# Kernel optimization log

Hardware: AMD Instinct MI355X
Metric: run time of the kernel (lower is better)

The kernel has to match this reference:

```python
import jax, jax.numpy as jnp
import numpy as np

N_NODES = 50000
N_EDGES = 800000
HEADS = 4
OUT_CH = 32
EDGE_EMB = 4
NEG_SLOPE = 0.2


def setup_inputs() -> dict:
    key = jax.random.key(0)
    ks = jax.random.split(key, 6)
    x = jax.random.normal(ks[0], (N_NODES, 128), dtype=jnp.float32)
    edge_index = jax.random.randint(ks[1], (2, N_EDGES), 0, N_NODES, dtype=jnp.int32)
    edge_attr = jax.random.normal(ks[2], (N_EDGES, 8), dtype=jnp.float32)
    W = jax.random.normal(ks[3], (128, HEADS * OUT_CH), dtype=jnp.float32) * 0.08
    We = jax.random.normal(ks[4], (8, HEADS * EDGE_EMB), dtype=jnp.float32) * 0.3
    att = jax.random.normal(ks[5], (1, HEADS, 2 * OUT_CH + EDGE_EMB), dtype=jnp.float32) * 0.1
    bias = jnp.zeros((HEADS * OUT_CH,), dtype=jnp.float32)
    return {"x": x, "edge_index": edge_index, "edge_attr": edge_attr,
            "W": W, "We": We, "att": att, "bias": bias}


def reference(x, edge_index, edge_attr, W, We, att, bias):
    # x: [N, Din], edge_index: [2, E] (row 0 = source j, row 1 = target i)
    src = edge_index[0]
    dst = edge_index[1]
    n = x.shape[0]

    xh = (x @ W).reshape(n, HEADS, OUT_CH)                    # [N, H, O]
    eh = (edge_attr @ We).reshape(-1, HEADS, EDGE_EMB)        # [E, H, P]

    a_i = att[0, :, :OUT_CH]                                  # [H, O]
    a_j = att[0, :, OUT_CH:2 * OUT_CH]                        # [H, O]
    a_e = att[0, :, 2 * OUT_CH:]                              # [H, P]

    # per-node dot with att halves, then gather per edge (avoids [E,H,O] concat)
    s_i = jnp.einsum('nho,ho->nh', xh, a_i)                   # [N, H]
    s_j = jnp.einsum('nho,ho->nh', xh, a_j)                   # [N, H]
    s_e = jnp.einsum('ehp,hp->eh', eh, a_e)                   # [E, H]

    alpha = s_i[dst] + s_j[src] + s_e                         # [E, H]
    alpha = jax.nn.leaky_relu(alpha, NEG_SLOPE)

    # segment softmax over incoming edges of each target node
    m = jax.ops.segment_max(alpha, dst, num_segments=n)       # [N, H]
    m = jnp.where(jnp.isfinite(m), m, 0.0)
    ea = jnp.exp(alpha - m[dst])                              # [E, H]
    denom = jax.ops.segment_sum(ea, dst, num_segments=n)      # [N, H]
    alpha = ea / (denom[dst] + 1e-16)                         # [E, H]

    msg = xh[src] * alpha[:, :, None]                         # [E, H, O]
    aggr = jax.ops.segment_sum(msg, dst, num_segments=n)      # [N, H, O]
    out = aggr.reshape(n, HEADS * OUT_CH) + bias              # concat heads
    return out
```

## Files before the change

kernel.cpp:

```cpp
#include <hip/hip_runtime.h>
#include <hip/hip_fp16.h>
#include <stdint.h>
#include <math.h>

#define NEG_SLOPE 0.2f

static __device__ __forceinline__ unsigned short f2bf(float f) {
    unsigned u = __float_as_uint(f);
    unsigned r = (u + 0x7FFFu + ((u >> 16) & 1u)) >> 16;
    return (unsigned short)r;
}
static __device__ __forceinline__ unsigned pack_h2(float a, float b) {
    __half2 h = __floats2half2_rn(a, b);
    return *(unsigned*)&h;
}

__global__ __launch_bounds__(256, 4) void k_gemm_scatter(
    const float* __restrict__ x, const float* __restrict__ W,
    const float* __restrict__ att, unsigned short* __restrict__ xh16,
    float* __restrict__ s_i, float* __restrict__ s_j, int n, int GB,
    const int* __restrict__ ei, const float* __restrict__ edge_attr,
    const float* __restrict__ We, int* __restrict__ cnt, int4* __restrict__ bucket,
    int slots, int E) {
    if (blockIdx.x >= GB) {
        __shared__ float ceS[32];
        int t = threadIdx.x;
        if (t < 32) {
            int k = t >> 2, h = t & 3;
            float s = 0.f;
            #pragma unroll
            for (int p = 0; p < 4; ++p)
                s += We[k * 16 + h * 4 + p] * att[h * 68 + 64 + p];
            ceS[t] = s;
        }
        __syncthreads();
        int e = (blockIdx.x - GB) * 256 + t;
        if (e < E) {
            float4 ea0 = *(const float4*)(edge_attr + (size_t)e * 8);
            float4 ea1 = *(const float4*)(edge_attr + (size_t)e * 8 + 4);
            float eav[8] = {ea0.x, ea0.y, ea0.z, ea0.w, ea1.x, ea1.y, ea1.z, ea1.w};
            float se[4];
            #pragma unroll
            for (int h = 0; h < 4; ++h) {
                float s = 0.f;
                #pragma unroll
                for (int k = 0; k < 8; ++k) s += eav[k] * ceS[k * 4 + h];
                se[h] = s;
            }
            int src = ei[e], dst = ei[E + e];
            int4 ent;
            ent.x = src;
            ent.y = (int)pack_h2(se[0], se[1]);
            ent.z = (int)pack_h2(se[2], se[3]);
            ent.w = 0;
            int p = atomicAdd(&cnt[dst], 1);
            if (p < slots) bucket[(size_t)dst * slots + p] = ent;
        }
        return;
    }
    __shared__ float wS[32 * 128];
    __shared__ float xS[64 * 32];
    int t = threadIdx.x;
    int c4 = t & 31;
    int rg = t >> 5;
    int r0 = blockIdx.x * 64;

    float acc[8][4];
    #pragma unroll
    for (int r = 0; r < 8; ++r)
        #pragma unroll
        for (int j = 0; j < 4; ++j) acc[r][j] = 0.f;

    for (int ch = 0; ch < 4; ++ch) {
        {
            const float4* Wv = (const float4*)(W + (size_t)ch * 32 * 128);
            #pragma unroll
            for (int i = 0; i < 4; ++i)
                ((float4*)wS)[t + i * 256] = Wv[t + i * 256];
        }
        #pragma unroll
        for (int i = 0; i < 2; ++i) {
            int idx = t + i * 256;
            int r = idx >> 3;
            int q = idx & 7;
            int row = r0 + r;
            float4 v = make_float4(0.f, 0.f, 0.f, 0.f);
            if (row < n) v = *(const float4*)(x + (size_t)row * 128 + ch * 32 + q * 4);
            ((float4*)xS)[idx] = v;
        }
        __syncthreads();
        #pragma unroll 1
        for (int q = 0; q < 8; ++q) {
            float wv[4][4];
            #pragma unroll
            for (int kk = 0; kk < 4; ++kk)
                #pragma unroll
                for (int j = 0; j < 4; ++j)
                    wv[kk][j] = wS[(4 * q + kk) * 128 + 32 * j + c4];
            #pragma unroll
            for (int r = 0; r < 8; ++r) {
                float4 xv = ((const float4*)xS)[(rg * 8 + r) * 8 + q];
                #pragma unroll
                for (int j = 0; j < 4; ++j)
                    acc[r][j] += xv.x * wv[0][j] + xv.y * wv[1][j]
                               + xv.z * wv[2][j] + xv.w * wv[3][j];
            }
        }
        __syncthreads();
    }

    float ai[4], aj[4];
    #pragma unroll
    for (int j = 0; j < 4; ++j) {
        ai[j] = att[j * 68 + c4];
        aj[j] = att[j * 68 + 32 + c4];
    }
    #pragma unroll 1
    for (int r = 0; r < 8; ++r) {
        int row = r0 + rg * 8 + r;
        bool ok = row < n;
        if (ok) {
            #pragma unroll
            for (int j = 0; j < 4; ++j)
                xh16[(size_t)row * 128 + c4 + 32 * j] = f2bf(acc[r][j]);
        }
        float p[8];
        #pragma unroll
        for (int j = 0; j < 4; ++j) {
            p[j] = acc[r][j] * ai[j];
            p[4 + j] = acc[r][j] * aj[j];
        }
        #pragma unroll
        for (int m = 1; m < 32; m <<= 1) {
            #pragma unroll
            for (int i = 0; i < 8; ++i) p[i] += __shfl_xor(p[i], m);
        }
        if (c4 == 0 && ok) {
            *(float4*)(s_i + (size_t)row * 4) = make_float4(p[0], p[1], p[2], p[3]);
            *(float4*)(s_j + (size_t)row * 4) = make_float4(p[4], p[5], p[6], p[7]);
        }
    }
}

__global__ __launch_bounds__(256) void k_aggr(
    const int* __restrict__ cnt, const int4* __restrict__ bucket, int slots,
    const float* __restrict__ s_i, const float* __restrict__ s_j,
    const unsigned* __restrict__ xh32, const float* __restrict__ bias,
    float* __restrict__ out, int n) {
    __shared__ float wbuf[4][64][4];
    __shared__ int sbuf[4][64];
    int wid = threadIdx.x >> 6;
    int l = threadIdx.x & 63;
    int node = blockIdx.x * 4 + wid;
    if (node >= n) return;
    int deg = cnt[node];
    deg = deg < slots ? deg : slots;
    float2 b = ((const float2*)bias)[l];
    float2* op = (float2*)(out + (size_t)node * 128);
    if (deg == 0) { op[l] = b; return; }

    float4 si4 = *(const float4*)(s_i + (size_t)node * 4);
    float lg[4];
    int src = 0;
    bool valid = l < deg;
    if (valid) {
        int4 ent = bucket[(size_t)node * slots + l];
        src = ent.x;
        float4 sj4 = *(const float4*)(s_j + (size_t)src * 4);
        __half2 se01 = *(__half2*)&ent.y;
        __half2 se23 = *(__half2*)&ent.z;
        float2 se01f = __half22float2(se01);
        float2 se23f = __half22float2(se23);
        float a;
        a = si4.x + sj4.x + se01f.x; lg[0] = a > 0.f ? a : NEG_SLOPE * a;
        a = si4.y + sj4.y + se01f.y; lg[1] = a > 0.f ? a : NEG_SLOPE * a;
        a = si4.z + sj4.z + se23f.x; lg[2] = a > 0.f ? a : NEG_SLOPE * a;
        a = si4.w + sj4.w + se23f.y; lg[3] = a > 0.f ? a : NEG_SLOPE * a;
    } else {
        lg[0] = lg[1] = lg[2] = lg[3] = -INFINITY;
    }
    float mx[4];
    #pragma unroll
    for (int h = 0; h < 4; ++h) mx[h] = lg[h];
    #pragma unroll
    for (int m = 1; m < 64; m <<= 1)
        #pragma unroll
        for (int h = 0; h < 4; ++h) mx[h] = fmaxf(mx[h], __shfl_xor(mx[h], m));
    float w[4], sm[4];
    #pragma unroll
    for (int h = 0; h < 4; ++h) {
        w[h] = valid ? __expf(lg[h] - mx[h]) : 0.f;
        sm[h] = w[h];
    }
    #pragma unroll
    for (int m = 1; m < 64; m <<= 1)
        #pragma unroll
        for (int h = 0; h < 4; ++h) sm[h] += __shfl_xor(sm[h], m);
    #pragma unroll
    for (int h = 0; h < 4; ++h) w[h] *= 1.f / (sm[h] + 1e-16f);

    *(float4*)&wbuf[wid][l][0] = make_float4(w[0], w[1], w[2], w[3]);
    sbuf[wid][l] = src;

    int hsel = l >> 4;
    float a0 = 0.f, a1 = 0.f;
    for (int j0 = 0; j0 < deg; j0 += 8) {
        int srcs[8];
        float ws[8];
        #pragma unroll
        for (int j = 0; j < 8; ++j) {
            int jj = j0 + j < deg ? j0 + j : 0;
            bool in = j0 + j < deg;
            srcs[j] = sbuf[wid][jj];
            ws[j] = in ? wbuf[wid][jj][hsel] : 0.f;
        }
        unsigned u[8];
        #pragma unroll
        for (int j = 0; j < 8; ++j) u[j] = xh32[(size_t)srcs[j] * 64 + l];
        #pragma unroll
        for (int j = 0; j < 8; ++j) {
            a0 += ws[j] * __uint_as_float(u[j] << 16);
            a1 += ws[j] * __uint_as_float(u[j] & 0xffff0000u);
        }
    }
    op[l] = make_float2(a0 + b.x, a1 + b.y);
}

extern "C" void kernel_launch(void* const* d_in, const int* in_sizes, int n_in,
                              void* d_out, int out_size, void* d_ws, size_t ws_size,
                              hipStream_t stream) {
    const float* x    = (const float*)d_in[0];
    const int*   ei   = (const int*)d_in[1];
    const float* eattr= (const float*)d_in[2];
    const float* W    = (const float*)d_in[3];
    const float* We   = (const float*)d_in[4];
    const float* att  = (const float*)d_in[5];
    const float* bias = (const float*)d_in[6];
    float* out = (float*)d_out;
    int n = in_sizes[0] / 128;
    int E = in_sizes[1] / 2;

    char* w = (char*)d_ws;
    auto alloc = [&](size_t bytes) {
        char* p = w;
        w += (bytes + 255) & ~(size_t)255;
        return (void*)p;
    };
    unsigned short* xh16 = (unsigned short*)alloc((size_t)n * 128 * 2);
    float* s_i           = (float*)alloc((size_t)n * 16);
    float* s_j           = (float*)alloc((size_t)n * 16);
    int* cnt             = (int*)alloc((size_t)n * 4);
    size_t remain = (ws_size > (size_t)(w - (char*)d_ws))
                  ? ws_size - (size_t)(w - (char*)d_ws) : 0;
    int slots = (int)(remain / ((size_t)n * 16));
    if (slots > 64) slots = 64;
    if (slots < 32) slots = 32;
    int4* bucket         = (int4*)alloc((size_t)n * slots * 16);

    int GB = (n + 63) / 64;
    int EB = (E + 255) / 256;

    (void)hipMemsetAsync(cnt, 0, (size_t)n * 4, stream);
    k_gemm_scatter<<<GB + EB, 256, 0, stream>>>(x, W, att, xh16, s_i, s_j, n, GB,
                                                ei, eattr, We, cnt, bucket, slots, E);
    k_aggr<<<(n + 3) / 4, 256, 0, stream>>>(cnt, bucket, slots, s_i, s_j,
                                            (const unsigned*)xh16, bias, out, n);
}
```

Baseline: 189.2 us.

## Scatter edge ids into buckets and store edge records contiguously

The edge pass now writes each edge's 16-byte record (source plus half-precision edge scores) coalesced by edge index, and scatters only a 4-byte edge id into the per-target bucket. The aggregation kernel reads the id and then gathers the record. The goal is to shrink the random scattered writes from 16 to 4 bytes per edge, at the cost of an extra dependent random 16-byte read in aggregation. The launch bound's minimum-blocks hint is also raised from 4 to 6, which limits registers for the GEMM path.

```diff
diff --git a/kernel.cpp b/kernel.cpp
--- a/kernel.cpp
+++ b/kernel.cpp
@@ -15,12 +15,13 @@
     return *(unsigned*)&h;
 }
 
-__global__ __launch_bounds__(256, 4) void k_gemm_scatter(
+__global__ __launch_bounds__(256, 6) void k_gemm_scatter(
     const float* __restrict__ x, const float* __restrict__ W,
     const float* __restrict__ att, unsigned short* __restrict__ xh16,
     float* __restrict__ s_i, float* __restrict__ s_j, int n, int GB,
     const int* __restrict__ ei, const float* __restrict__ edge_attr,
-    const float* __restrict__ We, int* __restrict__ cnt, int4* __restrict__ bucket,
+    const float* __restrict__ We, int* __restrict__ cnt,
+    int* __restrict__ bucket4, int4* __restrict__ erec,
     int slots, int E) {
     if (blockIdx.x >= GB) {
         __shared__ float ceS[32];
@@ -48,13 +49,14 @@
                 se[h] = s;
             }
             int src = ei[e], dst = ei[E + e];
-            int4 ent;
-            ent.x = src;
-            ent.y = (int)pack_h2(se[0], se[1]);
-            ent.z = (int)pack_h2(se[2], se[3]);
-            ent.w = 0;
+            int4 rec;
+            rec.x = src;
+            rec.y = (int)pack_h2(se[0], se[1]);
+            rec.z = (int)pack_h2(se[2], se[3]);
+            rec.w = 0;
+            erec[e] = rec;
             int p = atomicAdd(&cnt[dst], 1);
-            if (p < slots) bucket[(size_t)dst * slots + p] = ent;
+            if (p < slots) bucket4[(size_t)dst * slots + p] = e;
         }
         return;
     }
@@ -143,7 +145,8 @@
 }
 
 __global__ __launch_bounds__(256) void k_aggr(
-    const int* __restrict__ cnt, const int4* __restrict__ bucket, int slots,
+    const int* __restrict__ cnt, const int* __restrict__ bucket4,
+    const int4* __restrict__ erec, int slots,
     const float* __restrict__ s_i, const float* __restrict__ s_j,
     const unsigned* __restrict__ xh32, const float* __restrict__ bias,
     float* __restrict__ out, int n) {
@@ -164,11 +167,12 @@
     int src = 0;
     bool valid = l < deg;
     if (valid) {
-        int4 ent = bucket[(size_t)node * slots + l];
-        src = ent.x;
+        int e = bucket4[(size_t)node * slots + l];
+        int4 rec = erec[e];
+        src = rec.x;
         float4 sj4 = *(const float4*)(s_j + (size_t)src * 4);
-        __half2 se01 = *(__half2*)&ent.y;
-        __half2 se23 = *(__half2*)&ent.z;
+        __half2 se01 = *(__half2*)&rec.y;
+        __half2 se23 = *(__half2*)&rec.z;
         float2 se01f = __half22float2(se01);
         float2 se23f = __half22float2(se23);
         float a;
@@ -250,19 +254,21 @@
     float* s_i           = (float*)alloc((size_t)n * 16);
     float* s_j           = (float*)alloc((size_t)n * 16);
     int* cnt             = (int*)alloc((size_t)n * 4);
+    int4* erec           = (int4*)alloc((size_t)E * 16);
     size_t remain = (ws_size > (size_t)(w - (char*)d_ws))
                   ? ws_size - (size_t)(w - (char*)d_ws) : 0;
-    int slots = (int)(remain / ((size_t)n * 16));
+    int slots = (int)(remain / ((size_t)n * 4));
     if (slots > 64) slots = 64;
     if (slots < 32) slots = 32;
-    int4* bucket         = (int4*)alloc((size_t)n * slots * 16);
+    int* bucket4         = (int*)alloc((size_t)n * slots * 4);
 
     int GB = (n + 63) / 64;
     int EB = (E + 255) / 256;
 
     (void)hipMemsetAsync(cnt, 0, (size_t)n * 4, stream);
     k_gemm_scatter<<<GB + EB, 256, 0, stream>>>(x, W, att, xh16, s_i, s_j, n, GB,
-                                                ei, eattr, We, cnt, bucket, slots, E);
-    k_aggr<<<(n + 3) / 4, 256, 0, stream>>>(cnt, bucket, slots, s_i, s_j,
+                                                ei, eattr, We, cnt, bucket4, erec,
+                                                slots, E);
+    k_aggr<<<(n + 3) / 4, 256, 0, stream>>>(cnt, bucket4, erec, slots, s_i, s_j,
                                             (const unsigned*)xh16, bias, out, n);
 }
```

After: 232.2 us. 1.23x slower.

## Give each GEMM thread four contiguous output columns to vectorize and shrink reductions

Applied to the files above, without the earlier changes.

Each thread in the node-projection GEMM now owns four adjacent output columns inside one head, not one column from each of the four heads. This lets W be read from shared memory as float4 vectors and lets the bf16 output be written as one 8-byte ushort4 store. Since a thread's columns now share a head, the attention dot products need a 3-step shuffle reduction over 8 lanes for 2 values, down from a 5-step reduction over 32 lanes for 8 values. The new float4 shared-memory reads may cause more LDS bank conflicts, and the s_i/s_j results are now written as scalar stores.

```diff
diff --git a/kernel.cpp b/kernel.cpp
--- a/kernel.cpp
+++ b/kernel.cpp
@@ -91,53 +91,54 @@
         __syncthreads();
         #pragma unroll 1
         for (int q = 0; q < 8; ++q) {
-            float wv[4][4];
-            #pragma unroll
-            for (int kk = 0; kk < 4; ++kk)
-                #pragma unroll
-                for (int j = 0; j < 4; ++j)
-                    wv[kk][j] = wS[(4 * q + kk) * 128 + 32 * j + c4];
+            float4 wv0 = *(const float4*)&wS[(4 * q + 0) * 128 + 4 * c4];
+            float4 wv1 = *(const float4*)&wS[(4 * q + 1) * 128 + 4 * c4];
+            float4 wv2 = *(const float4*)&wS[(4 * q + 2) * 128 + 4 * c4];
+            float4 wv3 = *(const float4*)&wS[(4 * q + 3) * 128 + 4 * c4];
             #pragma unroll
             for (int r = 0; r < 8; ++r) {
                 float4 xv = ((const float4*)xS)[(rg * 8 + r) * 8 + q];
-                #pragma unroll
-                for (int j = 0; j < 4; ++j)
-                    acc[r][j] += xv.x * wv[0][j] + xv.y * wv[1][j]
-                               + xv.z * wv[2][j] + xv.w * wv[3][j];
+                acc[r][0] += xv.x * wv0.x + xv.y * wv1.x + xv.z * wv2.x + xv.w * wv3.x;
+                acc[r][1] += xv.x * wv0.y + xv.y * wv1.y + xv.z * wv2.y + xv.w * wv3.y;
+                acc[r][2] += xv.x * wv0.z + xv.y * wv1.z + xv.z * wv2.z + xv.w * wv3.z;
+                acc[r][3] += xv.x * wv0.w + xv.y * wv1.w + xv.z * wv2.w + xv.w * wv3.w;
             }
         }
         __syncthreads();
     }
 
+    int h = c4 >> 3;
+    int cb = 4 * (c4 & 7);
     float ai[4], aj[4];
     #pragma unroll
     for (int j = 0; j < 4; ++j) {
-        ai[j] = att[j * 68 + c4];
-        aj[j] = att[j * 68 + 32 + c4];
+        ai[j] = att[h * 68 + cb + j];
+        aj[j] = att[h * 68 + 32 + cb + j];
     }
     #pragma unroll 1
     for (int r = 0; r < 8; ++r) {
         int row = r0 + rg * 8 + r;
         bool ok = row < n;
         if (ok) {
-            #pragma unroll
-            for (int j = 0; j < 4; ++j)
-                xh16[(size_t)row * 128 + c4 + 32 * j] = f2bf(acc[r][j]);
-        }
-        float p[8];
-        #pragma unroll
-        for (int j = 0; j < 4; ++j) {
-            p[j] = acc[r][j] * ai[j];
-            p[4 + j] = acc[r][j] * aj[j];
-        }
-        #pragma unroll
-        for (int m = 1; m < 32; m <<= 1) {
-            #pragma unroll
-            for (int i = 0; i < 8; ++i) p[i] += __shfl_xor(p[i], m);
-        }
-        if (c4 == 0 && ok) {
-            *(float4*)(s_i + (size_t)row * 4) = make_float4(p[0], p[1], p[2], p[3]);
-            *(float4*)(s_j + (size_t)row * 4) = make_float4(p[4], p[5], p[6], p[7]);
+            ushort4 us;
+            us.x = f2bf(acc[r][0]);
+            us.y = f2bf(acc[r][1]);
+            us.z = f2bf(acc[r][2]);
+            us.w = f2bf(acc[r][3]);
+            *(ushort4*)(xh16 + (size_t)row * 128 + 4 * c4) = us;
+        }
+        float pi = acc[r][0] * ai[0] + acc[r][1] * ai[1]
+                 + acc[r][2] * ai[2] + acc[r][3] * ai[3];
+        float pj = acc[r][0] * aj[0] + acc[r][1] * aj[1]
+                 + acc[r][2] * aj[2] + acc[r][3] * aj[3];
+        #pragma unroll
+        for (int m = 1; m < 8; m <<= 1) {
+            pi += __shfl_xor(pi, m);
+            pj += __shfl_xor(pj, m);
+        }
+        if ((c4 & 7) == 0 && ok) {
+            s_i[(size_t)row * 4 + h] = pi;
+            s_j[(size_t)row * 4 + h] = pj;
         }
     }
 }
```

After: 190.1 us, median of 2. No clear change (+0.5%).
